# Optimization experiments

Measured on AMD Instinct MI355X. Metric: run time of the kernel, lower is better.

The kernel has to match this reference:

```python
import jax, jax.numpy as jnp
import numpy as np

# dims: batch, tokens, model dim, heads, head_dim, context len, n_blocks, ffn dim
B, L, D, H, HD, S, NB, DFF = 1, 3072, 1024, 16, 64, 512, 2, 4096
T3, H3, W3 = 12, 16, 16  # latent video grid, T3*H3*W3 == L


def _ln(x):
    # LayerNorm, elementwise_affine=False, eps=1e-6
    m = jnp.mean(x, axis=-1, keepdims=True)
    v = jnp.mean(jnp.square(x - m), axis=-1, keepdims=True)
    return (x - m) * jax.lax.rsqrt(v + 1e-6)


def _rot_half(x):
    x1, x2 = jnp.split(x, 2, axis=-1)
    return jnp.concatenate([-x2, x1], axis=-1)


def _rope3d(head_dim, t, h, w):
    d = head_dim // 6
    def band(n):
        freqs = 1.0 / 10000.0 ** (np.arange(0, 2 * d, 2, dtype=np.float32) / (2 * d))
        return np.outer(np.arange(n, dtype=np.float32), freqs)  # [n, d]
    te, he, we = band(t), band(h), band(w)
    rope = np.zeros((t, h, w, head_dim), dtype=np.float32)
    rope[:, :, :, :d] = te[:, None, None, :]
    rope[:, :, :, d:2 * d] = he[None, :, None, :]
    rope[:, :, :, 2 * d:3 * d] = we[None, None, :, :]
    return jnp.asarray(rope.reshape(t * h * w, head_dim))


def _forward(x, timestep_emb, context_emb, rope_emb, adaW, adab, sqW, skW, svW,
             soW, sob, cqW, ckW, cvW, coW, cob, f1W, f1b, f2W, f2b):
    Bv, Lv, Dv = x.shape
    hd = rope_emb.shape[-1]
    nh = Dv // hd
    scale = hd ** -0.5
    cos = jnp.cos(rope_emb)[None, None]  # [1,1,L,hd]
    sin = jnp.sin(rope_emb)[None, None]

    def heads(y):  # [B,N,D] -> [B,H,N,hd]
        return y.reshape(Bv, -1, nh, hd).transpose(0, 2, 1, 3)

    def merge(y):  # [B,H,L,hd] -> [B,L,D]
        return y.transpose(0, 2, 1, 3).reshape(Bv, Lv, Dv)

    for i in range(adaW.shape[0]):
        mods = timestep_emb @ adaW[i].T + adab[i]  # [B, 6D]
        sh_msa, sc_msa, g_msa, sh_mlp, sc_mlp, g_mlp = jnp.split(mods, 6, axis=-1)
        # --- AdaLN + self-attention with RoPE ---
        hx = _ln(x) * (1.0 + sc_msa[:, None, :]) + sh_msa[:, None, :]
        q, k, v = heads(hx @ sqW[i].T), heads(hx @ skW[i].T), heads(hx @ svW[i].T)
        q = q * cos + _rot_half(q) * sin
        k = k * cos + _rot_half(k) * sin
        a = jax.nn.softmax(jnp.einsum('bhld,bhmd->bhlm', q, k) * scale, axis=-1)
        o = merge(jnp.einsum('bhlm,bhmd->bhld', a, v))
        x = x + g_msa[:, None, :] * (o @ soW[i].T + sob[i])
        # --- cross-attention (no gate, no modulation) ---
        hx = _ln(x)
        q = heads(hx @ cqW[i].T)
        k = heads(context_emb @ ckW[i].T)
        v = heads(context_emb @ cvW[i].T)
        a = jax.nn.softmax(jnp.einsum('bhld,bhsd->bhls', q, k) * scale, axis=-1)
        o = merge(jnp.einsum('bhls,bhsd->bhld', a, v))
        x = x + (o @ coW[i].T + cob[i])
        # --- AdaLN + MLP (exact GELU) ---
        hx = _ln(x) * (1.0 + sc_mlp[:, None, :]) + sh_mlp[:, None, :]
        hx = jax.nn.gelu(hx @ f1W[i].T + f1b[i], approximate=False)
        x = x + g_mlp[:, None, :] * (hx @ f2W[i].T + f2b[i])
    return x


def setup_inputs() -> dict:
    ks = jax.random.split(jax.random.key(0), 20)
    s = 0.02
    return {
        'x': jax.random.normal(ks[0], (B, L, D), jnp.float32),
        'timestep_emb': jax.random.normal(ks[1], (B, D), jnp.float32),
        'context_emb': jax.random.normal(ks[2], (B, S, D), jnp.float32),
        'rope_emb': _rope3d(HD, T3, H3, W3),
        'adaW': jax.random.normal(ks[3], (NB, 6 * D, D), jnp.float32) * s,
        'adab': jnp.zeros((NB, 6 * D), jnp.float32),
        'sqW': jax.random.normal(ks[4], (NB, D, D), jnp.float32) * s,
        'skW': jax.random.normal(ks[5], (NB, D, D), jnp.float32) * s,
        'svW': jax.random.normal(ks[6], (NB, D, D), jnp.float32) * s,
        'soW': jax.random.normal(ks[7], (NB, D, D), jnp.float32) * s,
        'sob': jnp.zeros((NB, D), jnp.float32),
        'cqW': jax.random.normal(ks[8], (NB, D, D), jnp.float32) * s,
        'ckW': jax.random.normal(ks[9], (NB, D, D), jnp.float32) * s,
        'cvW': jax.random.normal(ks[10], (NB, D, D), jnp.float32) * s,
        'coW': jax.random.normal(ks[11], (NB, D, D), jnp.float32) * s,
        'cob': jnp.zeros((NB, D), jnp.float32),
        'f1W': jax.random.normal(ks[12], (NB, DFF, D), jnp.float32) * s,
        'f1b': jnp.zeros((NB, DFF), jnp.float32),
        'f2W': jax.random.normal(ks[13], (NB, D, DFF), jnp.float32) * s,
        'f2b': jnp.zeros((NB, D), jnp.float32),
    }


def reference(x, timestep_emb, context_emb, rope_emb, adaW, adab, sqW, skW, svW,
              soW, sob, cqW, ckW, cvW, coW, cob, f1W, f1b, f2W, f2b):
    return _forward(x, timestep_emb, context_emb, rope_emb, adaW, adab, sqW, skW,
                    svW, soW, sob, cqW, ckW, cvW, coW, cob, f1W, f1b, f2W, f2b)
```

## Files before the change

kernel.cpp:

```cpp
#include <hip/hip_runtime.h>
#include <math.h>

typedef __attribute__((ext_vector_type(8))) short bf16x8;
typedef __attribute__((ext_vector_type(4))) float f32x4;
typedef unsigned short u16;
typedef unsigned int u32;

#define DEV static __device__ __forceinline__

typedef __attribute__((address_space(3))) u32 lds_u32;
typedef const __attribute__((address_space(1))) u32 glb_u32;

DEV void gload16(const void* g, void* l){
  __builtin_amdgcn_global_load_lds((glb_u32*)g, (lds_u32*)l, 16, 0, 0);
}

DEV u16 f2bf(float f){
  u32 u = __builtin_bit_cast(u32, f);
  u32 r = (u + 0x7fffu + ((u >> 16) & 1u)) >> 16;
  return (u16)r;
}
DEV float bf2f(u16 h){
  u32 u = ((u32)h) << 16;
  return __builtin_bit_cast(float, u);
}
DEV u32 pack2(float a, float b){
  u32 ua = (__builtin_bit_cast(u32, a) + 0x8000u) >> 16;
  u32 ub = (__builtin_bit_cast(u32, b) + 0x8000u) & 0xffff0000u;
  return ua | ub;
}
DEV float gelu_exact(float x){ return 0.5f*x*(1.f+erff(x*0.70710678118654752f)); }

DEV void xcd_remap(int &bx, int &by){
  int gx = gridDim.x, gy = gridDim.y;
  int n = gx*gy;
  if ((n & 7) == 0){
    int id = by*gx + bx;
    int q = n >> 3;
    int sid = (id & 7)*q + (id >> 3);
    bx = sid % gx;
    by = sid / gx;
  }
}

__global__ __launch_bounds__(256) void k_copy_f32(const float* __restrict__ in, float* __restrict__ out, int n4){
  int i = blockIdx.x*256 + threadIdx.x;
  if (i < n4) ((float4*)out)[i] = ((const float4*)in)[i];
}

__global__ __launch_bounds__(256) void k_cvt_bf16(const float* __restrict__ in, u16* __restrict__ out, int n4){
  int i = blockIdx.x*256 + threadIdx.x;
  if (i < n4){
    float4 v = ((const float4*)in)[i];
    ushort4 o;
    o.x = f2bf(v.x); o.y = f2bf(v.y); o.z = f2bf(v.z); o.w = f2bf(v.w);
    ((ushort4*)out)[i] = o;
  }
}

__global__ __launch_bounds__(256) void k_ada(const float* __restrict__ te,
    const float* __restrict__ adaW, const float* __restrict__ adab,
    float* __restrict__ mods){
  int row = blockIdx.x*4 + (threadIdx.x>>6);
  int lane = threadIdx.x & 63;
  const float* wr = adaW + (size_t)row*1024;
  float s = 0.f;
  #pragma unroll
  for (int j=0; j<4; j++){
    int c = lane*4 + j*256;
    float4 a = *(const float4*)(te + c);
    float4 b = *(const float4*)(wr + c);
    s += a.x*b.x + a.y*b.y + a.z*b.z + a.w*b.w;
  }
  #pragma unroll
  for (int off=32; off; off>>=1) s += __shfl_down(s, off);
  if (!lane) mods[row] = s + adab[row];
}

__global__ __launch_bounds__(256) void k_ln_mod(const float* __restrict__ x,
    const float* __restrict__ sh, const float* __restrict__ sc,
    u16* __restrict__ out){
  int row = blockIdx.x, t = threadIdx.x;
  const float* xr = x + (size_t)row*1024;
  float4 v = ((const float4*)xr)[t];
  float s  = v.x+v.y+v.z+v.w;
  float sq = v.x*v.x+v.y*v.y+v.z*v.z+v.w*v.w;
  #pragma unroll
  for (int off=32; off; off>>=1){ s += __shfl_down(s,off); sq += __shfl_down(sq,off); }
  __shared__ float red[8];
  int w = t>>6, lane = t&63;
  if (!lane){ red[w] = s; red[4+w] = sq; }
  __syncthreads();
  s  = red[0]+red[1]+red[2]+red[3];
  sq = red[4]+red[5]+red[6]+red[7];
  float mean = s*(1.f/1024.f);
  float var  = sq*(1.f/1024.f) - mean*mean;
  float rst  = rsqrtf(var + 1e-6f);
  float vv[4] = {v.x, v.y, v.z, v.w};
  ushort4 o;
  u16 ob[4];
  #pragma unroll
  for (int j=0;j<4;j++){
    int col = t*4+j;
    float y = (vv[j]-mean)*rst;
    if (sh) y = y*(1.f + sc[col]) + sh[col];
    ob[j] = f2bf(y);
  }
  o.x=ob[0]; o.y=ob[1]; o.z=ob[2]; o.w=ob[3];
  *(ushort4*)(out + (size_t)row*1024 + t*4) = o;
}

__global__ __launch_bounds__(256) void k_rope(u16* __restrict__ q, u16* __restrict__ k,
    const float* __restrict__ rope){
  int idx = blockIdx.x*256 + threadIdx.x;
  int d = idx & 31;
  int h = (idx >> 5) & 15;
  int p = idx >> 9;
  const float* rr = rope + (size_t)p*64;
  float a0 = rr[d], a1 = rr[d+32];
  float c0 = cosf(a0), s0 = sinf(a0);
  float c1 = cosf(a1), s1 = sinf(a1);
  size_t o = (size_t)p*1024 + h*64 + d;
  float q0 = bf2f(q[o]), q1 = bf2f(q[o+32]);
  q[o]    = f2bf((q0*c0 - q1*s0)*0.125f);
  q[o+32] = f2bf((q1*c1 + q0*s1)*0.125f);
  float k0 = bf2f(k[o]), k1 = bf2f(k[o+32]);
  k[o]    = f2bf(k0*c0 - k1*s0);
  k[o+32] = f2bf(k1*c1 + k0*s1);
}

DEV void gemm_loop(const u16* __restrict__ X, const u16* __restrict__ W,
                   int bm, int bn, int K, u16* As, u16* Bs, f32x4 acc[4][4])
{
  int t = threadIdx.x;
  int w = t>>6, lane = t&63;
  int wr = (w>>1)*64, wc = (w&1)*64;
  int fr = lane&15, g = lane>>4;
  int arow = lane>>2, acol = (lane&3)*8;
  const u16* xp = X + (size_t)(bm + w*32 + arow)*K + acol;
  const u16* wp = W + (size_t)(bn + w*32 + arow)*K + acol;
  int nk = K >> 5;
  {
    u16* a = As + w*1024; u16* b = Bs + w*1024;
    gload16(xp, a);             gload16(xp + (size_t)16*K, a + 512);
    gload16(wp, b);             gload16(wp + (size_t)16*K, b + 512);
  }
  for (int kt = 0; kt < nk; ++kt){
    __syncthreads();
    int cur = kt & 1;
    if (kt + 1 < nk){
      int nb = cur ^ 1;
      int k0 = (kt+1) << 5;
      u16* a = As + nb*4096 + w*1024; u16* b = Bs + nb*4096 + w*1024;
      gload16(xp + k0, a);        gload16(xp + k0 + (size_t)16*K, a + 512);
      gload16(wp + k0, b);        gload16(wp + k0 + (size_t)16*K, b + 512);
    }
    const u16* ab = As + cur*4096;
    const u16* bb = Bs + cur*4096;
    bf16x8 a[4], b[4];
    #pragma unroll
    for (int i=0;i<4;i++) a[i] = *(const bf16x8*)(ab + (wr+i*16+fr)*32 + g*8);
    #pragma unroll
    for (int i=0;i<4;i++) b[i] = *(const bf16x8*)(bb + (wc+i*16+fr)*32 + g*8);
    #pragma unroll
    for (int i=0;i<4;i++)
      #pragma unroll
      for (int j=0;j<4;j++)
        acc[i][j] = __builtin_amdgcn_mfma_f32_16x16x32_bf16(a[i], b[j], acc[i][j], 0, 0, 0);
  }
}

template<int EPI>
__global__ __launch_bounds__(256) void k_gemm_bf16(
    const u16* __restrict__ X, const u16* __restrict__ W,
    const float* __restrict__ bias,
    u16* __restrict__ Yout,
    const float* __restrict__ resin, float* __restrict__ resout,
    const float* __restrict__ gate,
    int M, int N, int K)
{
  __shared__ __align__(16) u16 As[2*128*32];
  __shared__ __align__(16) u16 Bs[2*128*32];
  int bx = blockIdx.x, by = blockIdx.y;
  xcd_remap(bx, by);
  int bm = bx*128, bn = by*128;
  f32x4 acc[4][4] = {};
  gemm_loop(X, W, bm, bn, K, As, Bs, acc);
  int lane = threadIdx.x & 63, w = threadIdx.x>>6;
  int wr = (w>>1)*64, wc = (w&1)*64;
  int fr = lane&15, g = lane>>4;
  #pragma unroll
  for (int i=0;i<4;i++){
    #pragma unroll
    for (int j=0;j<4;j++){
      int col = bn + wc + j*16 + fr;
      float bv = bias ? bias[col] : 0.f;
      #pragma unroll
      for (int r=0;r<4;r++){
        int row = bm + wr + i*16 + g*4 + r;
        float y = acc[i][j][r] + bv;
        if (EPI == 1){
          Yout[(size_t)row*N + col] = f2bf(gelu_exact(y));
        } else if (EPI == 2){
          float gt = gate ? gate[col] : 1.f;
          resout[(size_t)row*N + col] = resin[(size_t)row*N + col] + gt*y;
        } else {
          Yout[(size_t)row*N + col] = f2bf(y*0.125f);
        }
      }
    }
  }
}

template<int MODE>
__global__ __launch_bounds__(256) void k_qkv(
    const u16* __restrict__ X,
    const u16* __restrict__ W0, const u16* __restrict__ W1, const u16* __restrict__ W2,
    u16* __restrict__ Y0, u16* __restrict__ Y1, u16* __restrict__ VT,
    int M, int ldvt)
{
  __shared__ __align__(16) u16 As[2*128*32];
  __shared__ __align__(16) u16 Bs[2*128*32];
  int bx = blockIdx.x, by = blockIdx.y;
  xcd_remap(bx, by);
  int bm = bx*128, bn = by*128;
  int sel = bn >> 10;
  int bnl = bn & 1023;
  const u16* W = (MODE==0) ? (sel==0 ? W0 : (sel==1 ? W1 : W2))
                           : (sel==0 ? W0 : W1);
  f32x4 acc[4][4] = {};
  {
    gemm_loop(X, W, bm, bnl, 1024, As, Bs, acc);
  }
  int lane = threadIdx.x & 63, w = threadIdx.x>>6;
  int wr = (w>>1)*64, wc = (w&1)*64;
  int fr = lane&15, g = lane>>4;
  const int lastSel = (MODE==0) ? 2 : 1;
  if (sel < lastSel){
    u16* Y = (sel==0) ? Y0 : Y1;
    #pragma unroll
    for (int i=0;i<4;i++)
      #pragma unroll
      for (int j=0;j<4;j++){
        int col = bnl + wc + j*16 + fr;
        #pragma unroll
        for (int r=0;r<4;r++){
          int row = bm + wr + i*16 + g*4 + r;
          Y[(size_t)row*1024 + col] = f2bf(acc[i][j][r]);
        }
      }
  } else {
    #pragma unroll
    for (int i=0;i<4;i++)
      #pragma unroll
      for (int j=0;j<4;j++){
        int col = bnl + wc + j*16 + fr;
        int row0 = bm + wr + i*16 + g*4;
        uint2 pk;
        pk.x = pack2(acc[i][j][0], acc[i][j][1]);
        pk.y = pack2(acc[i][j][2], acc[i][j][3]);
        *(uint2*)(VT + (size_t)col*ldvt + row0) = pk;
      }
  }
}

template<int EPI>
__global__ __launch_bounds__(256) void k_gemm_f32(
    const u16* __restrict__ X, const float* __restrict__ W,
    const float* __restrict__ bias,
    u16* __restrict__ Yout,
    const float* __restrict__ resin, float* __restrict__ resout,
    const float* __restrict__ gate,
    int M, int N, int K)
{
  __shared__ __align__(16) u16 As[128][32];
  __shared__ __align__(16) u16 Bs[128][40];
  int bx = blockIdx.x, by = blockIdx.y;
  xcd_remap(bx, by);
  int bm = bx*128, bn = by*128;
  int t = threadIdx.x;
  int w = t>>6, lane = t&63;
  int wr = (w>>1)*64, wc = (w&1)*64;
  int fr = lane&15, g = lane>>4;
  f32x4 acc[4][4] = {};
  int arow = lane>>2, acol = (lane&3)*8;
  int srow = t>>2, scol = (t&3)*8;
  for (int k0=0; k0<K; k0+=32){
    #pragma unroll
    for (int inst=0; inst<2; ++inst){
      int r = w*32 + inst*16 + arow;
      gload16(X + (size_t)(bm+r)*K + k0 + acol, &As[w*32+inst*16][0]);
    }
    #pragma unroll
    for (int it=0; it<2; ++it){
      const float* wp = W + (size_t)(bn+srow+it*64)*K + k0 + scol;
      float4 f0 = *(const float4*)(wp);
      float4 f1 = *(const float4*)(wp+4);
      uint4 bw;
      bw.x = (u32)f2bf(f0.x) | ((u32)f2bf(f0.y)<<16);
      bw.y = (u32)f2bf(f0.z) | ((u32)f2bf(f0.w)<<16);
      bw.z = (u32)f2bf(f1.x) | ((u32)f2bf(f1.y)<<16);
      bw.w = (u32)f2bf(f1.z) | ((u32)f2bf(f1.w)<<16);
      *(uint4*)&Bs[srow+it*64][scol] = bw;
    }
    __syncthreads();
    bf16x8 a[4], b[4];
    #pragma unroll
    for (int i=0;i<4;i++) a[i] = *(const bf16x8*)&As[wr+i*16+fr][g*8];
    #pragma unroll
    for (int i=0;i<4;i++) b[i] = *(const bf16x8*)&Bs[wc+i*16+fr][g*8];
    #pragma unroll
    for (int i=0;i<4;i++)
      #pragma unroll
      for (int j=0;j<4;j++)
        acc[i][j] = __builtin_amdgcn_mfma_f32_16x16x32_bf16(a[i], b[j], acc[i][j], 0, 0, 0);
    __syncthreads();
  }
  #pragma unroll
  for (int i=0;i<4;i++){
    #pragma unroll
    for (int j=0;j<4;j++){
      int col = bn + wc + j*16 + fr;
      float bv = bias ? bias[col] : 0.f;
      #pragma unroll
      for (int r=0;r<4;r++){
        int row = bm + wr + i*16 + g*4 + r;
        float y = acc[i][j][r] + bv;
        if (EPI == 0){
          Yout[(size_t)row*N + col] = f2bf(y);
        } else if (EPI == 1){
          Yout[(size_t)row*N + col] = f2bf(gelu_exact(y));
        } else if (EPI == 2){
          float gt = gate ? gate[col] : 1.f;
          resout[(size_t)row*N + col] = resin[(size_t)row*N + col] + gt*y;
        } else if (EPI == 3){
          Yout[(size_t)col*M + row] = f2bf(y);
        } else {
          Yout[(size_t)row*N + col] = f2bf(y*0.125f);
        }
      }
    }
  }
}

__global__ __launch_bounds__(256) void k_flash(
    const u16* __restrict__ Q, const u16* __restrict__ Kb, const u16* __restrict__ VT,
    u16* __restrict__ O, int Lkv)
{
  __shared__ __align__(16) u16 Ks[2*64*64];
  __shared__ __align__(16) u16 Vs[2*64*64];
  __shared__ __align__(16) u16 Ps[4][16][72];
  int bx = blockIdx.x, by = blockIdx.y;
  xcd_remap(bx, by);
  int h = by;
  int q0 = bx*64;
  int t = threadIdx.x, w = t>>6, lane = t&63;
  int fr = lane&15, g = lane>>4;
  const u16* qrow = Q + (size_t)(q0 + w*16 + fr)*1024 + h*64;
  bf16x8 aq0 = *(const bf16x8*)(qrow + g*8);
  bf16x8 aq1 = *(const bf16x8*)(qrow + 32 + g*8);
  f32x4 accO[4] = {};
  float m = -1e30f, l = 0.f;
  int slot = lane & 7, rop = lane >> 3;
  const u16* kbase = Kb + (size_t)h*64;
  const u16* vbase = VT + (size_t)h*64*Lkv;
  int nt = Lkv >> 6;
  {
    #pragma unroll
    for (int inst=0; inst<2; ++inst){
      int row = w*16 + inst*8 + rop;
      int ss = slot ^ (row & 7);
      gload16(kbase + (size_t)row*1024 + ss*8, Ks + (w*16+inst*8)*64);
      gload16(vbase + (size_t)row*Lkv + ss*8, Vs + (w*16+inst*8)*64);
    }
  }
  for (int tt=0; tt<nt; ++tt){
    __syncthreads();
    int cur = tt & 1;
    if (tt+1 < nt){
      int nb = cur ^ 1;
      int k0 = (tt+1) << 6;
      #pragma unroll
      for (int inst=0; inst<2; ++inst){
        int row = w*16 + inst*8 + rop;
        int ss = slot ^ (row & 7);
        gload16(kbase + (size_t)(k0+row)*1024 + ss*8, Ks + nb*4096 + (w*16+inst*8)*64);
        gload16(vbase + (size_t)row*Lkv + k0 + ss*8, Vs + nb*4096 + (w*16+inst*8)*64);
      }
    }
    const u16* kc = Ks + cur*4096;
    const u16* vc = Vs + cur*4096;
    f32x4 st[4] = {};
    #pragma unroll
    for (int kb=0;kb<4;kb++){
      int rowK = kb*16 + fr;
      bf16x8 b0 = *(const bf16x8*)(kc + rowK*64 + ((g  ) ^ (rowK&7))*8);
      bf16x8 b1 = *(const bf16x8*)(kc + rowK*64 + ((4+g) ^ (rowK&7))*8);
      st[kb] = __builtin_amdgcn_mfma_f32_16x16x32_bf16(b0, aq0, st[kb], 0,0,0);
      st[kb] = __builtin_amdgcn_mfma_f32_16x16x32_bf16(b1, aq1, st[kb], 0,0,0);
    }
    float x[16];
    #pragma unroll
    for (int kb=0;kb<4;kb++)
      #pragma unroll
      for (int r=0;r<4;r++) x[kb*4+r] = st[kb][r];
    float tmax = x[0];
    #pragma unroll
    for (int ii=1; ii<16; ii++) tmax = fmaxf(tmax, x[ii]);
    tmax = fmaxf(tmax, __shfl_xor(tmax, 16));
    tmax = fmaxf(tmax, __shfl_xor(tmax, 32));
    if (!__all(tmax <= m + 8.f)){
      float mn = fmaxf(m, tmax);
      float er = __expf(m - mn);
      m = mn;
      l *= er;
      #pragma unroll
      for (int r=0;r<4;r++){
        float erq = __shfl(er, g*4+r);
        #pragma unroll
        for (int nd=0; nd<4; nd++) accO[nd][r] *= erq;
      }
    }
    float ts = 0.f;
    u32 pk[8];
    #pragma unroll
    for (int kb=0;kb<4;kb++){
      float p0 = __expf(x[kb*4+0] - m);
      float p1 = __expf(x[kb*4+1] - m);
      float p2 = __expf(x[kb*4+2] - m);
      float p3 = __expf(x[kb*4+3] - m);
      ts += (p0+p1)+(p2+p3);
      pk[kb*2]   = pack2(p0,p1);
      pk[kb*2+1] = pack2(p2,p3);
    }
    ts += __shfl_xor(ts, 16);
    ts += __shfl_xor(ts, 32);
    l += ts;
    #pragma unroll
    for (int kb=0;kb<4;kb++){
      uint2 pv; pv.x = pk[kb*2]; pv.y = pk[kb*2+1];
      *(uint2*)&Ps[w][fr][kb*16 + g*4] = pv;
    }
    bf16x8 ap0 = *(const bf16x8*)&Ps[w][fr][g*8];
    bf16x8 ap1 = *(const bf16x8*)&Ps[w][fr][32 + g*8];
    #pragma unroll
    for (int nd=0; nd<4; nd++){
      int rowV = nd*16 + fr;
      bf16x8 b0 = *(const bf16x8*)(vc + rowV*64 + ((g  ) ^ (rowV&7))*8);
      bf16x8 b1 = *(const bf16x8*)(vc + rowV*64 + ((4+g) ^ (rowV&7))*8);
      accO[nd] = __builtin_amdgcn_mfma_f32_16x16x32_bf16(ap0, b0, accO[nd], 0,0,0);
      accO[nd] = __builtin_amdgcn_mfma_f32_16x16x32_bf16(ap1, b1, accO[nd], 0,0,0);
    }
  }
  float rl = 1.f / l;
  #pragma unroll
  for (int r=0;r<4;r++){
    float rlq = __shfl(rl, g*4+r);
    int row = q0 + w*16 + g*4 + r;
    #pragma unroll
    for (int nd=0; nd<4; nd++)
      O[(size_t)row*1024 + h*64 + nd*16 + fr] = f2bf(accO[nd][r] * rlq);
  }
}

extern "C" void kernel_launch(void* const* d_in, const int* in_sizes, int n_in,
                              void* d_out, int out_size, void* d_ws, size_t ws_size,
                              hipStream_t stream){
  const float* x_in = (const float*)d_in[0];
  const float* te   = (const float*)d_in[1];
  const float* ctx  = (const float*)d_in[2];
  const float* rope = (const float*)d_in[3];
  const float* adaW = (const float*)d_in[4];
  const float* adab = (const float*)d_in[5];
  const float* sqW  = (const float*)d_in[6];
  const float* skW  = (const float*)d_in[7];
  const float* svW  = (const float*)d_in[8];
  const float* soW  = (const float*)d_in[9];
  const float* sob  = (const float*)d_in[10];
  const float* cqW  = (const float*)d_in[11];
  const float* ckW  = (const float*)d_in[12];
  const float* cvW  = (const float*)d_in[13];
  const float* coW  = (const float*)d_in[14];
  const float* cob  = (const float*)d_in[15];
  const float* f1W  = (const float*)d_in[16];
  const float* f1b  = (const float*)d_in[17];
  const float* f2W  = (const float*)d_in[18];
  const float* f2b  = (const float*)d_in[19];
  float* x = (float*)d_out;

  char* p = (char*)d_ws;
  size_t used = 0;
  auto alloc = [&](size_t bytes){
    void* r = (void*)(p + used);
    used += (bytes + 255) & ~(size_t)255;
    return r;
  };
  u16* hx   = (u16*)alloc((size_t)3072*1024*2);
  u16* qb   = (u16*)alloc((size_t)3072*1024*2);
  u16* kb   = (u16*)alloc((size_t)3072*1024*2);
  u16* vt   = (u16*)alloc((size_t)1024*3072*2);
  u16* ob   = (u16*)alloc((size_t)3072*1024*2);
  u16* mid  = (u16*)alloc((size_t)3072*4096*2);
  u16* ctxb = (u16*)alloc((size_t)512*1024*2);
  float* mods = (float*)alloc((size_t)2*6144*4);
  size_t base_used = used;
  const size_t NW_SMALL = (size_t)2*1024*1024;
  const size_t NW_BIG   = (size_t)2*4096*1024;
  size_t wbytes = (8*NW_SMALL + 2*NW_BIG)*2;
  bool pre = (base_used + wbytes + 4096) <= ws_size;

  u16 *sqWb=nullptr,*skWb=nullptr,*svWb=nullptr,*soWb=nullptr,
      *cqWb=nullptr,*ckWb=nullptr,*cvWb=nullptr,*coWb=nullptr,
      *f1Wb=nullptr,*f2Wb=nullptr;
  if (pre){
    sqWb=(u16*)alloc(NW_SMALL*2); skWb=(u16*)alloc(NW_SMALL*2);
    svWb=(u16*)alloc(NW_SMALL*2); soWb=(u16*)alloc(NW_SMALL*2);
    cqWb=(u16*)alloc(NW_SMALL*2); ckWb=(u16*)alloc(NW_SMALL*2);
    cvWb=(u16*)alloc(NW_SMALL*2); coWb=(u16*)alloc(NW_SMALL*2);
    f1Wb=(u16*)alloc(NW_BIG*2);   f2Wb=(u16*)alloc(NW_BIG*2);
    auto CVT = [&](const float* s, u16* d, size_t n){
      k_cvt_bf16<<<(int)(n/1024), 256, 0, stream>>>(s, d, (int)(n/4));
    };
    CVT(sqW,sqWb,NW_SMALL); CVT(skW,skWb,NW_SMALL);
    CVT(svW,svWb,NW_SMALL); CVT(soW,soWb,NW_SMALL);
    CVT(cqW,cqWb,NW_SMALL); CVT(ckW,ckWb,NW_SMALL);
    CVT(cvW,cvWb,NW_SMALL); CVT(coW,coWb,NW_SMALL);
    CVT(f1W,f1Wb,NW_BIG);   CVT(f2W,f2Wb,NW_BIG);
  }

  k_copy_f32<<<3072, 256, 0, stream>>>(x_in, x, 786432);
  k_cvt_bf16<<<512, 256, 0, stream>>>(ctx, ctxb, 131072);
  k_ada<<<3072, 256, 0, stream>>>(te, adaW, adab, mods);

  for (int i=0; i<2; ++i){
    const float* mi = mods + (size_t)i*6144;
    size_t wo = (size_t)i*1024*1024;
    size_t wof = (size_t)i*4096*1024;
    k_ln_mod<<<3072,256,0,stream>>>(x, mi+0, mi+1024, hx);
    if (pre){
      k_qkv<0><<<dim3(24,24),256,0,stream>>>(hx, sqWb+wo, skWb+wo, svWb+wo, qb, kb, vt, 3072, 3072);
    } else {
      k_gemm_f32<0><<<dim3(24,8),256,0,stream>>>(hx, sqW+wo, nullptr, qb, nullptr,nullptr,nullptr, 3072,1024,1024);
      k_gemm_f32<0><<<dim3(24,8),256,0,stream>>>(hx, skW+wo, nullptr, kb, nullptr,nullptr,nullptr, 3072,1024,1024);
      k_gemm_f32<3><<<dim3(24,8),256,0,stream>>>(hx, svW+wo, nullptr, vt, nullptr,nullptr,nullptr, 3072,1024,1024);
    }
    k_rope<<<6144,256,0,stream>>>(qb, kb, rope);
    k_flash<<<dim3(48,16),256,0,stream>>>(qb, kb, vt, ob, 3072);
    if (pre)
      k_gemm_bf16<2><<<dim3(24,8),256,0,stream>>>(ob, soWb+wo, sob+(size_t)i*1024, nullptr, x, x, mi+2048, 3072,1024,1024);
    else
      k_gemm_f32<2><<<dim3(24,8),256,0,stream>>>(ob, soW+wo, sob+(size_t)i*1024, nullptr, x, x, mi+2048, 3072,1024,1024);
    k_ln_mod<<<3072,256,0,stream>>>(x, nullptr, nullptr, hx);
    if (pre){
      k_gemm_bf16<4><<<dim3(24,8),256,0,stream>>>(hx, cqWb+wo, nullptr, qb, nullptr,nullptr,nullptr, 3072,1024,1024);
      k_qkv<1><<<dim3(4,16),256,0,stream>>>(ctxb, ckWb+wo, cvWb+wo, nullptr, kb, nullptr, vt, 512, 512);
    } else {
      k_gemm_f32<4><<<dim3(24,8),256,0,stream>>>(hx, cqW+wo, nullptr, qb, nullptr,nullptr,nullptr, 3072,1024,1024);
      k_gemm_f32<0><<<dim3(4,8),256,0,stream>>>(ctxb, ckW+wo, nullptr, kb, nullptr,nullptr,nullptr, 512,1024,1024);
      k_gemm_f32<3><<<dim3(4,8),256,0,stream>>>(ctxb, cvW+wo, nullptr, vt, nullptr,nullptr,nullptr, 512,1024,1024);
    }
    k_flash<<<dim3(48,16),256,0,stream>>>(qb, kb, vt, ob, 512);
    if (pre)
      k_gemm_bf16<2><<<dim3(24,8),256,0,stream>>>(ob, coWb+wo, cob+(size_t)i*1024, nullptr, x, x, nullptr, 3072,1024,1024);
    else
      k_gemm_f32<2><<<dim3(24,8),256,0,stream>>>(ob, coW+wo, cob+(size_t)i*1024, nullptr, x, x, nullptr, 3072,1024,1024);
    k_ln_mod<<<3072,256,0,stream>>>(x, mi+3072, mi+4096, hx);
    if (pre){
      k_gemm_bf16<1><<<dim3(24,32),256,0,stream>>>(hx, f1Wb+wof, f1b+(size_t)i*4096, mid, nullptr,nullptr,nullptr, 3072,4096,1024);
      k_gemm_bf16<2><<<dim3(24,8),256,0,stream>>>(mid, f2Wb+wof, f2b+(size_t)i*1024, nullptr, x, x, mi+5120, 3072,1024,4096);
    } else {
      k_gemm_f32<1><<<dim3(24,32),256,0,stream>>>(hx, f1W+wof, f1b+(size_t)i*4096, mid, nullptr,nullptr,nullptr, 3072,4096,1024);
      k_gemm_f32<2><<<dim3(24,8),256,0,stream>>>(mid, f2W+wof, f2b+(size_t)i*1024, nullptr, x, x, mi+5120, 3072,1024,4096);
    }
  }
}
```

Before: 948.1 us.

## Split-K the N=1024 GEMMs, fold log2e into Q scale, add MFMA setprio

Adds a split-K GEMM kernel that writes fp32 partial sums to a workspace, plus a reduce kernel that applies bias, gate and residual (or the Q scale). The output-projection, cross-attention Q and FFN2 GEMMs use it, raising the block count from 192 to 384 or 768 on a GPU with many CUs. The Q scale now includes log2(e), so flash attention can use exp2f and a rescale threshold adjusted to match. s_setprio is wrapped around the MFMA loops in the GEMM and flash kernels. The trade-off is extra partial-sum memory traffic and an extra kernel launch per split GEMM.

```diff
diff --git a/kernel.cpp b/kernel.cpp
--- a/kernel.cpp
+++ b/kernel.cpp
@@ -30,6 +30,8 @@
   return ua | ub;
 }
 DEV float gelu_exact(float x){ return 0.5f*x*(1.f+erff(x*0.70710678118654752f)); }
+
+#define QSCALE 0.18033688f
 
 DEV void xcd_remap(int &bx, int &by){
   int gx = gridDim.x, gy = gridDim.y;
@@ -122,28 +124,28 @@
   float c1 = cosf(a1), s1 = sinf(a1);
   size_t o = (size_t)p*1024 + h*64 + d;
   float q0 = bf2f(q[o]), q1 = bf2f(q[o+32]);
-  q[o]    = f2bf((q0*c0 - q1*s0)*0.125f);
-  q[o+32] = f2bf((q1*c1 + q0*s1)*0.125f);
+  q[o]    = f2bf((q0*c0 - q1*s0)*QSCALE);
+  q[o+32] = f2bf((q1*c1 + q0*s1)*QSCALE);
   float k0 = bf2f(k[o]), k1 = bf2f(k[o+32]);
   k[o]    = f2bf(k0*c0 - k1*s0);
   k[o+32] = f2bf(k1*c1 + k0*s1);
 }
 
 DEV void gemm_loop(const u16* __restrict__ X, const u16* __restrict__ W,
-                   int bm, int bn, int K, u16* As, u16* Bs, f32x4 acc[4][4])
+                   int bm, int bn, int ld, int lenK, u16* As, u16* Bs, f32x4 acc[4][4])
 {
   int t = threadIdx.x;
   int w = t>>6, lane = t&63;
   int wr = (w>>1)*64, wc = (w&1)*64;
   int fr = lane&15, g = lane>>4;
   int arow = lane>>2, acol = (lane&3)*8;
-  const u16* xp = X + (size_t)(bm + w*32 + arow)*K + acol;
-  const u16* wp = W + (size_t)(bn + w*32 + arow)*K + acol;
-  int nk = K >> 5;
+  const u16* xp = X + (size_t)(bm + w*32 + arow)*ld + acol;
+  const u16* wp = W + (size_t)(bn + w*32 + arow)*ld + acol;
+  int nk = lenK >> 5;
   {
     u16* a = As + w*1024; u16* b = Bs + w*1024;
-    gload16(xp, a);             gload16(xp + (size_t)16*K, a + 512);
-    gload16(wp, b);             gload16(wp + (size_t)16*K, b + 512);
+    gload16(xp, a);             gload16(xp + (size_t)16*ld, a + 512);
+    gload16(wp, b);             gload16(wp + (size_t)16*ld, b + 512);
   }
   for (int kt = 0; kt < nk; ++kt){
     __syncthreads();
@@ -152,8 +154,8 @@
       int nb = cur ^ 1;
       int k0 = (kt+1) << 5;
       u16* a = As + nb*4096 + w*1024; u16* b = Bs + nb*4096 + w*1024;
-      gload16(xp + k0, a);        gload16(xp + k0 + (size_t)16*K, a + 512);
-      gload16(wp + k0, b);        gload16(wp + k0 + (size_t)16*K, b + 512);
+      gload16(xp + k0, a);        gload16(xp + k0 + (size_t)16*ld, a + 512);
+      gload16(wp + k0, b);        gload16(wp + k0 + (size_t)16*ld, b + 512);
     }
     const u16* ab = As + cur*4096;
     const u16* bb = Bs + cur*4096;
@@ -162,11 +164,13 @@
     for (int i=0;i<4;i++) a[i] = *(const bf16x8*)(ab + (wr+i*16+fr)*32 + g*8);
     #pragma unroll
     for (int i=0;i<4;i++) b[i] = *(const bf16x8*)(bb + (wc+i*16+fr)*32 + g*8);
+    __builtin_amdgcn_s_setprio(1);
     #pragma unroll
     for (int i=0;i<4;i++)
       #pragma unroll
       for (int j=0;j<4;j++)
         acc[i][j] = __builtin_amdgcn_mfma_f32_16x16x32_bf16(a[i], b[j], acc[i][j], 0, 0, 0);
+    __builtin_amdgcn_s_setprio(0);
   }
 }
 
@@ -185,7 +189,7 @@
   xcd_remap(bx, by);
   int bm = bx*128, bn = by*128;
   f32x4 acc[4][4] = {};
-  gemm_loop(X, W, bm, bn, K, As, Bs, acc);
+  gemm_loop(X, W, bm, bn, K, K, As, Bs, acc);
   int lane = threadIdx.x & 63, w = threadIdx.x>>6;
   int wr = (w>>1)*64, wc = (w&1)*64;
   int fr = lane&15, g = lane>>4;
@@ -205,10 +209,77 @@
           float gt = gate ? gate[col] : 1.f;
           resout[(size_t)row*N + col] = resin[(size_t)row*N + col] + gt*y;
         } else {
-          Yout[(size_t)row*N + col] = f2bf(y*0.125f);
+          Yout[(size_t)row*N + col] = f2bf(y*QSCALE);
         }
       }
     }
+  }
+}
+
+__global__ __launch_bounds__(256) void k_gemm_part(
+    const u16* __restrict__ X, const u16* __restrict__ W,
+    float* __restrict__ pp, int M, int N, int K, int Ks)
+{
+  __shared__ __align__(16) u16 As[2*128*32];
+  __shared__ __align__(16) u16 Bs[2*128*32];
+  int bx = blockIdx.x, by = blockIdx.y;
+  xcd_remap(bx, by);
+  int s = blockIdx.z;
+  int bm = bx*128, bn = by*128;
+  f32x4 acc[4][4] = {};
+  gemm_loop(X + (size_t)s*Ks, W + (size_t)s*Ks, bm, bn, K, Ks, As, Bs, acc);
+  float* out = pp + (size_t)s*M*N;
+  int lane = threadIdx.x & 63, w = threadIdx.x>>6;
+  int wr = (w>>1)*64, wc = (w&1)*64;
+  int fr = lane&15, g = lane>>4;
+  #pragma unroll
+  for (int i=0;i<4;i++)
+    #pragma unroll
+    for (int j=0;j<4;j++){
+      int col = bn + wc + j*16 + fr;
+      #pragma unroll
+      for (int r=0;r<4;r++){
+        int row = bm + wr + i*16 + g*4 + r;
+        out[(size_t)row*N + col] = acc[i][j][r];
+      }
+    }
+}
+
+template<int EPI>
+__global__ __launch_bounds__(256) void k_reduce(
+    const float* __restrict__ pp, int S, const float* __restrict__ bias,
+    const float* __restrict__ resin, float* __restrict__ resout,
+    const float* __restrict__ gate, u16* __restrict__ Ybf,
+    int MN, int N)
+{
+  int idx = blockIdx.x*256 + threadIdx.x;
+  int base = idx*4;
+  if (base >= MN) return;
+  float4 s4 = *(const float4*)(pp + base);
+  for (int s=1; s<S; ++s){
+    float4 t4 = *(const float4*)(pp + (size_t)s*MN + base);
+    s4.x += t4.x; s4.y += t4.y; s4.z += t4.z; s4.w += t4.w;
+  }
+  int col = base & (N-1);
+  float b0=0,b1=0,b2=0,b3=0;
+  if (bias){ b0=bias[col]; b1=bias[col+1]; b2=bias[col+2]; b3=bias[col+3]; }
+  if (EPI == 2){
+    float g0=1,g1=1,g2=1,g3=1;
+    if (gate){ g0=gate[col]; g1=gate[col+1]; g2=gate[col+2]; g3=gate[col+3]; }
+    float4 rv = *(const float4*)(resin + base);
+    float4 o;
+    o.x = rv.x + g0*(s4.x+b0);
+    o.y = rv.y + g1*(s4.y+b1);
+    o.z = rv.z + g2*(s4.z+b2);
+    o.w = rv.w + g3*(s4.w+b3);
+    *(float4*)(resout + base) = o;
+  } else {
+    ushort4 o;
+    o.x = f2bf((s4.x+b0)*QSCALE);
+    o.y = f2bf((s4.y+b1)*QSCALE);
+    o.z = f2bf((s4.z+b2)*QSCALE);
+    o.w = f2bf((s4.w+b3)*QSCALE);
+    *(ushort4*)(Ybf + base) = o;
   }
 }
 
@@ -229,9 +300,7 @@
   const u16* W = (MODE==0) ? (sel==0 ? W0 : (sel==1 ? W1 : W2))
                            : (sel==0 ? W0 : W1);
   f32x4 acc[4][4] = {};
-  {
-    gemm_loop(X, W, bm, bnl, 1024, As, Bs, acc);
-  }
+  gemm_loop(X, W, bm, bnl, 1024, 1024, As, Bs, acc);
   int lane = threadIdx.x & 63, w = threadIdx.x>>6;
   int wr = (w>>1)*64, wc = (w&1)*64;
   int fr = lane&15, g = lane>>4;
@@ -336,7 +405,7 @@
         } else if (EPI == 3){
           Yout[(size_t)col*M + row] = f2bf(y);
         } else {
-          Yout[(size_t)row*N + col] = f2bf(y*0.125f);
+          Yout[(size_t)row*N + col] = f2bf(y*QSCALE);
         }
       }
     }
@@ -391,6 +460,7 @@
     const u16* kc = Ks + cur*4096;
     const u16* vc = Vs + cur*4096;
     f32x4 st[4] = {};
+    __builtin_amdgcn_s_setprio(1);
     #pragma unroll
     for (int kb=0;kb<4;kb++){
       int rowK = kb*16 + fr;
@@ -399,6 +469,7 @@
       st[kb] = __builtin_amdgcn_mfma_f32_16x16x32_bf16(b0, aq0, st[kb], 0,0,0);
       st[kb] = __builtin_amdgcn_mfma_f32_16x16x32_bf16(b1, aq1, st[kb], 0,0,0);
     }
+    __builtin_amdgcn_s_setprio(0);
     float x[16];
     #pragma unroll
     for (int kb=0;kb<4;kb++)
@@ -409,9 +480,9 @@
     for (int ii=1; ii<16; ii++) tmax = fmaxf(tmax, x[ii]);
     tmax = fmaxf(tmax, __shfl_xor(tmax, 16));
     tmax = fmaxf(tmax, __shfl_xor(tmax, 32));
-    if (!__all(tmax <= m + 8.f)){
-      float mn = fmaxf(m, tmax);
-      float er = __expf(m - mn);
+    if (!__all(tmax <= m + 11.5416f)){
+    float mn = fmaxf(m, tmax);
+      float er = exp2f(m - mn);
       m = mn;
       l *= er;
       #pragma unroll
@@ -425,10 +496,10 @@
     u32 pk[8];
     #pragma unroll
     for (int kb=0;kb<4;kb++){
-      float p0 = __expf(x[kb*4+0] - m);
-      float p1 = __expf(x[kb*4+1] - m);
-      float p2 = __expf(x[kb*4+2] - m);
-      float p3 = __expf(x[kb*4+3] - m);
+      float p0 = exp2f(x[kb*4+0] - m);
+      float p1 = exp2f(x[kb*4+1] - m);
+      float p2 = exp2f(x[kb*4+2] - m);
+      float p3 = exp2f(x[kb*4+3] - m);
       ts += (p0+p1)+(p2+p3);
       pk[kb*2]   = pack2(p0,p1);
       pk[kb*2+1] = pack2(p2,p3);
@@ -443,6 +514,7 @@
     }
     bf16x8 ap0 = *(const bf16x8*)&Ps[w][fr][g*8];
     bf16x8 ap1 = *(const bf16x8*)&Ps[w][fr][32 + g*8];
+    __builtin_amdgcn_s_setprio(1);
     #pragma unroll
     for (int nd=0; nd<4; nd++){
       int rowV = nd*16 + fr;
@@ -451,6 +523,7 @@
       accO[nd] = __builtin_amdgcn_mfma_f32_16x16x32_bf16(ap0, b0, accO[nd], 0,0,0);
       accO[nd] = __builtin_amdgcn_mfma_f32_16x16x32_bf16(ap1, b1, accO[nd], 0,0,0);
     }
+    __builtin_amdgcn_s_setprio(0);
   }
   float rl = 1.f / l;
   #pragma unroll
@@ -527,6 +600,11 @@
     CVT(cvW,cvWb,NW_SMALL); CVT(coW,coWb,NW_SMALL);
     CVT(f1W,f1Wb,NW_BIG);   CVT(f2W,f2Wb,NW_BIG);
   }
+  const size_t PPN = (size_t)4*3072*1024;
+  float* pp = nullptr;
+  bool splitok = pre && (used + PPN*4 + 4096) <= ws_size;
+  if (splitok) pp = (float*)alloc(PPN*4);
+  const int MN = 3072*1024;
 
   k_copy_f32<<<3072, 256, 0, stream>>>(x_in, x, 786432);
   k_cvt_bf16<<<512, 256, 0, stream>>>(ctx, ctxb, 131072);
@@ -546,12 +624,19 @@
     }
     k_rope<<<6144,256,0,stream>>>(qb, kb, rope);
     k_flash<<<dim3(48,16),256,0,stream>>>(qb, kb, vt, ob, 3072);
-    if (pre)
+    if (splitok){
+      k_gemm_part<<<dim3(24,8,2),256,0,stream>>>(ob, soWb+wo, pp, 3072,1024,1024,512);
+      k_reduce<2><<<3072,256,0,stream>>>(pp, 2, sob+(size_t)i*1024, x, x, mi+2048, nullptr, MN, 1024);
+    } else if (pre)
       k_gemm_bf16<2><<<dim3(24,8),256,0,stream>>>(ob, soWb+wo, sob+(size_t)i*1024, nullptr, x, x, mi+2048, 3072,1024,1024);
     else
       k_gemm_f32<2><<<dim3(24,8),256,0,stream>>>(ob, soW+wo, sob+(size_t)i*1024, nullptr, x, x, mi+2048, 3072,1024,1024);
     k_ln_mod<<<3072,256,0,stream>>>(x, nullptr, nullptr, hx);
-    if (pre){
+    if (splitok){
+      k_gemm_part<<<dim3(24,8,2),256,0,stream>>>(hx, cqWb+wo, pp, 3072,1024,1024,512);
+      k_reduce<4><<<3072,256,0,stream>>>(pp, 2, nullptr, nullptr, nullptr, nullptr, qb, MN, 1024);
+      k_qkv<1><<<dim3(4,16),256,0,stream>>>(ctxb, ckWb+wo, cvWb+wo, nullptr, kb, nullptr, vt, 512, 512);
+    } else if (pre){
       k_gemm_bf16<4><<<dim3(24,8),256,0,stream>>>(hx, cqWb+wo, nullptr, qb, nullptr,nullptr,nullptr, 3072,1024,1024);
       k_qkv<1><<<dim3(4,16),256,0,stream>>>(ctxb, ckWb+wo, cvWb+wo, nullptr, kb, nullptr, vt, 512, 512);
     } else {
@@ -560,17 +645,25 @@
       k_gemm_f32<3><<<dim3(4,8),256,0,stream>>>(ctxb, cvW+wo, nullptr, vt, nullptr,nullptr,nullptr, 512,1024,1024);
     }
     k_flash<<<dim3(48,16),256,0,stream>>>(qb, kb, vt, ob, 512);
-    if (pre)
+    if (splitok){
+      k_gemm_part<<<dim3(24,8,2),256,0,stream>>>(ob, coWb+wo, pp, 3072,1024,1024,512);
+      k_reduce<2><<<3072,256,0,stream>>>(pp, 2, cob+(size_t)i*1024, x, x, nullptr, nullptr, MN, 1024);
+    } else if (pre)
       k_gemm_bf16<2><<<dim3(24,8),256,0,stream>>>(ob, coWb+wo, cob+(size_t)i*1024, nullptr, x, x, nullptr, 3072,1024,1024);
     else
       k_gemm_f32<2><<<dim3(24,8),256,0,stream>>>(ob, coW+wo, cob+(size_t)i*1024, nullptr, x, x, nullptr, 3072,1024,1024);
     k_ln_mod<<<3072,256,0,stream>>>(x, mi+3072, mi+4096, hx);
     if (pre){
       k_gemm_bf16<1><<<dim3(24,32),256,0,stream>>>(hx, f1Wb+wof, f1b+(size_t)i*4096, mid, nullptr,nullptr,nullptr, 3072,4096,1024);
-      k_gemm_bf16<2><<<dim3(24,8),256,0,stream>>>(mid, f2Wb+wof, f2b+(size_t)i*1024, nullptr, x, x, mi+5120, 3072,1024,4096);
     } else {
       k_gemm_f32<1><<<dim3(24,32),256,0,stream>>>(hx, f1W+wof, f1b+(size_t)i*4096, mid, nullptr,nullptr,nullptr, 3072,4096,1024);
+    }
+    if (splitok){
+      k_gemm_part<<<dim3(24,8,4),256,0,stream>>>(mid, f2Wb+wof, pp, 3072,1024,4096,1024);
+      k_reduce<2><<<3072,256,0,stream>>>(pp, 4, f2b+(size_t)i*1024, x, x, mi+5120, nullptr, MN, 1024);
+    } else if (pre)
+      k_gemm_bf16<2><<<dim3(24,8),256,0,stream>>>(mid, f2Wb+wof, f2b+(size_t)i*1024, nullptr, x, x, mi+5120, 3072,1024,4096);
+    else
       k_gemm_f32<2><<<dim3(24,8),256,0,stream>>>(mid, f2W+wof, f2b+(size_t)i*1024, nullptr, x, x, mi+5120, 3072,1024,4096);
-    }
-  }
-}
+  }
+}
```

Result: faster. 854.8 us (-9.8%).
